# Optimization experiments

Measured on AMD Instinct MI355X. Metric: run time of the kernel, lower is better.

Reference implementation:

```python
import jax, jax.numpy as jnp
import numpy as np

TEMPERATURE = 0.5  # init temperature; attn_drop=0.0 so dropout is identity


def setup_inputs() -> dict:
    key = jax.random.key(0)
    k1, k2, k3 = jax.random.split(key, 3)
    B, H, N, D = 4, 8, 2048, 64
    q = jax.random.normal(k1, (B, H, N, D), dtype=jnp.float32)
    k = jax.random.normal(k2, (B, H, N, D), dtype=jnp.float32)
    v = jax.random.normal(k3, (B, H, N, D), dtype=jnp.float32)
    scale = jnp.asarray(D ** -0.5, dtype=jnp.float32)
    return {"q": q, "k": k, "v": v, "scale": scale}


def reference(q, k, v, scale):
    # logits: [B,H,N,N]
    logits = jnp.einsum("bhqd,bhkd->bhqk", q, k) * scale
    # first softmax acts as a soft mask over keys
    soft_mask = jax.nn.softmax(logits / TEMPERATURE, axis=-1)
    # second softmax over masked logits (elementwise product, NOT matmul)
    attn = jax.nn.softmax(logits * soft_mask, axis=-1)
    # dropout with p=0.0 is identity
    out = jnp.einsum("bhqk,bhkd->bhqd", attn, v)
    return out
```

## Files before the change

### kernel.cpp

```cpp
#include <hip/hip_runtime.h>


typedef _Float16 f16;
typedef f16 f16x8 __attribute__((ext_vector_type(8)));
typedef f16 f16x4 __attribute__((ext_vector_type(4)));
typedef float f32x4 __attribute__((ext_vector_type(4)));

#define MFMA32(a, b, c) __builtin_amdgcn_mfma_f32_16x16x32_f16((a), (b), (c), 0, 0, 0)
#define MFMA16(a, b, c) __builtin_amdgcn_mfma_f32_16x16x16f16((a), (b), (c), 0, 0, 0)
#define EXP2(x) __builtin_amdgcn_exp2f(x)

#define N_CTX 2048
#define DH 64
#define KT 64
#define NKT (N_CTX / KT)
#define ROWS 128
#define QS 72

#define C2 2.885390081777927f

__device__ inline unsigned pk(float a, float b) {
    typedef __fp16 fp16x2_t __attribute__((ext_vector_type(2)));
    union { fp16x2_t v; unsigned u; } x;
    x.v = __builtin_amdgcn_cvt_pkrtz(a, b);
    return x.u;
}

__global__ __launch_bounds__(512, 4)
void stk_attn_mfma(const float* __restrict__ qg, const float* __restrict__ kg,
                   const float* __restrict__ vglob, const float* __restrict__ sg,
                   float* __restrict__ og) {
    __shared__ f16 Ks[2][KT * QS];
    __shared__ f16 Vt[2][DH * QS];

    const int tid  = threadIdx.x;
    const int wv   = tid >> 6;
    const int lane = tid & 63;
    const int l15  = lane & 15;
    const int q4   = lane >> 4;
    const int vp   = tid & 31;
    const int vgr  = tid >> 5;
    const int bh   = blockIdx.x & 31;
    const int q0   = (blockIdx.x >> 5) * ROWS;
    const float scale2 = sg[0] * C2;

    const float* qb = qg + (size_t)bh * N_CTX * DH;
    const float* kb = kg + (size_t)bh * N_CTX * DH;
    const float* vb = vglob + (size_t)bh * N_CTX * DH;
    float*       ob = og + (size_t)bh * N_CTX * DH;

    f16x8 aq[2];
    {
        const float* qrow = qb + (size_t)(q0 + wv * 16 + l15) * DH;
        #pragma unroll
        for (int kc = 0; kc < 2; ++kc) {
            float4 a0 = *(const float4*)&qrow[kc * 32 + q4 * 8];
            float4 a1 = *(const float4*)&qrow[kc * 32 + q4 * 8 + 4];
            union { f16x8 h; unsigned u[4]; } A;
            A.u[0] = pk(a0.x * scale2, a0.y * scale2);
            A.u[1] = pk(a0.z * scale2, a0.w * scale2);
            A.u[2] = pk(a1.x * scale2, a1.y * scale2);
            A.u[3] = pk(a1.z * scale2, a1.w * scale2);
            aq[kc] = A.h;
        }
    }

    int kofs[2], gofs[2];
    #pragma unroll
    for (int it = 0; it < 2; ++it) {
        int idx = it * 512 + tid;
        gofs[it] = (idx >> 4) * DH + (idx & 15) * 4;
        kofs[it] = (idx >> 4) * QS + (idx & 15) * 4;
    }
    const int c2p = ((vp >> 1) & 3) * 16 + (vp >> 3) * 4 + (vp & 1) * 2;

    f16* const ks_w  = &Ks[0][0];
    const f16* const ks_r = &Ks[0][l15 * QS + q4 * 8];
    f16* const vt_w  = &Vt[0][(vgr * 4) * QS + c2p];
    const f16* const vt_r = &Vt[0][l15 * QS + q4 * 16];
    const int KSB = KT * QS;

    float s1 = 0.f;
    float4 kr[2];
    #pragma unroll
    for (int it = 0; it < 2; ++it)
        kr[it] = *(const float4*)&kb[gofs[it]];
    #pragma unroll
    for (int it = 0; it < 2; ++it)
        *(uint2*)&ks_w[kofs[it]] =
            make_uint2(pk(kr[it].x, kr[it].y), pk(kr[it].z, kr[it].w));
    #pragma unroll
    for (int it = 0; it < 2; ++it)
        kr[it] = *(const float4*)&kb[KT * DH + gofs[it]];
    __syncthreads();

    for (int kt = 0; kt < NKT; ++kt) {
        const int cur = (kt & 1) * KSB, nxt = KSB - cur;
        #pragma unroll
        for (int it = 0; it < 2; ++it)
            *(uint2*)&ks_w[nxt + kofs[it]] =
                make_uint2(pk(kr[it].x, kr[it].y), pk(kr[it].z, kr[it].w));
        {
            int tn = (kt + 2 < NKT) ? kt + 2 : NKT - 1;
            #pragma unroll
            for (int it = 0; it < 2; ++it)
                kr[it] = *(const float4*)&kb[(size_t)tn * KT * DH + gofs[it]];
        }
        __builtin_amdgcn_s_setprio(1);
        #pragma unroll
        for (int kgi = 0; kgi < 4; ++kgi) {
            f16x8 b0 = *(const f16x8*)&ks_r[cur + kgi * 16 * QS];
            f16x8 b1 = *(const f16x8*)&ks_r[cur + kgi * 16 * QS + 32];
            f32x4 acc = {0.f, 0.f, 0.f, 0.f};
            acc = MFMA32(b0, aq[0], acc);
            acc = MFMA32(b1, aq[1], acc);
            s1 += (EXP2(acc[0]) + EXP2(acc[1])) + (EXP2(acc[2]) + EXP2(acc[3]));
        }
        __builtin_amdgcn_s_setprio(0);
        __syncthreads();
    }
    s1 += __shfl_xor(s1, 16, 64);
    s1 += __shfl_xor(s1, 32, 64);
    const float inv1 = 0.5f / s1;

    f32x4 O[4];
    #pragma unroll
    for (int dt = 0; dt < 4; ++dt) O[dt] = (f32x4){0.f, 0.f, 0.f, 0.f};
    f32x4 Oe = {0.f, 0.f, 0.f, 0.f};
    const f16x4 ones = {(f16)1.f, (f16)1.f, (f16)1.f, (f16)1.f};

    float4 vr0, vr2;
    #pragma unroll
    for (int it = 0; it < 2; ++it)
        kr[it] = *(const float4*)&kb[gofs[it]];
    #pragma unroll
    for (int it = 0; it < 2; ++it)
        *(uint2*)&ks_w[kofs[it]] =
            make_uint2(pk(kr[it].x, kr[it].y), pk(kr[it].z, kr[it].w));
    {
        const float* vs = vb + ((size_t)2 * vp) * DH + vgr * 4;
        float4 a0 = *(const float4*)(vs);
        float4 b0 = *(const float4*)(vs + DH);
        #pragma unroll
        for (int j = 0; j < 4; ++j)
            *(unsigned*)&vt_w[j * QS] = pk(((const float*)&a0)[j], ((const float*)&b0)[j]);
        const float* vs1 = vb + ((size_t)(KT + 2 * vp)) * DH + vgr * 4;
        vr0 = *(const float4*)(vs1);
        vr2 = *(const float4*)(vs1 + DH);
    }
    #pragma unroll
    for (int it = 0; it < 2; ++it)
        kr[it] = *(const float4*)&kb[KT * DH + gofs[it]];
    __syncthreads();

    for (int kt = 0; kt < NKT; ++kt) {
        const int cur = (kt & 1) * KSB, nxt = KSB - cur;
        #pragma unroll
        for (int it = 0; it < 2; ++it)
            *(uint2*)&ks_w[nxt + kofs[it]] =
                make_uint2(pk(kr[it].x, kr[it].y), pk(kr[it].z, kr[it].w));
        #pragma unroll
        for (int j = 0; j < 4; ++j)
            *(unsigned*)&vt_w[nxt + j * QS] =
                pk(((const float*)&vr0)[j], ((const float*)&vr2)[j]);
        {
            int tn = (kt + 2 < NKT) ? kt + 2 : NKT - 1;
            #pragma unroll
            for (int it = 0; it < 2; ++it)
                kr[it] = *(const float4*)&kb[(size_t)tn * KT * DH + gofs[it]];
            const float* vs = vb + ((size_t)(tn * KT + 2 * vp)) * DH + vgr * 4;
            vr0 = *(const float4*)(vs);
            vr2 = *(const float4*)(vs + DH);
        }
        __builtin_amdgcn_s_setprio(1);
        #pragma unroll
        for (int p = 0; p < 2; ++p) {
            f16x4 pfr[2];
            #pragma unroll
            for (int h = 0; h < 2; ++h) {
                const int kgi = p * 2 + h;
                f16x8 b0 = *(const f16x8*)&ks_r[cur + kgi * 16 * QS];
                f16x8 b1 = *(const f16x8*)&ks_r[cur + kgi * 16 * QS + 32];
                f32x4 acc = {0.f, 0.f, 0.f, 0.f};
                acc = MFMA32(b0, aq[0], acc);
                acc = MFMA32(b1, aq[1], acc);
                float e2r[4];
                #pragma unroll
                for (int r = 0; r < 4; ++r) {
                    float a  = acc[r];
                    float e1 = EXP2(a);
                    e2r[r] = EXP2((a * e1) * inv1);
                }
                union { f16x4 hh; unsigned u[2]; } P;
                P.u[0] = pk(e2r[0], e2r[1]);
                P.u[1] = pk(e2r[2], e2r[3]);
                pfr[h] = P.hh;
                Oe = MFMA16(ones, pfr[h], Oe);
            }
            #pragma unroll
            for (int dt = 0; dt < 4; ++dt) {
                f16x8 av = *(const f16x8*)&vt_r[cur + dt * 16 * QS + p * 8];
                f16x4 alo = __builtin_shufflevector(av, av, 0, 1, 2, 3);
                f16x4 ahi = __builtin_shufflevector(av, av, 4, 5, 6, 7);
                O[dt] = MFMA16(alo, pfr[0], O[dt]);
                O[dt] = MFMA16(ahi, pfr[1], O[dt]);
            }
        }
        __builtin_amdgcn_s_setprio(0);
        __syncthreads();
    }

    const float invl2 = 1.0f / Oe[0];
    const size_t orow = (size_t)(q0 + wv * 16 + l15) * DH;
    #pragma unroll
    for (int dt = 0; dt < 4; ++dt) {
        float4 o;
        o.x = O[dt][0] * invl2;
        o.y = O[dt][1] * invl2;
        o.z = O[dt][2] * invl2;
        o.w = O[dt][3] * invl2;
        *(float4*)&ob[orow + dt * 16 + q4 * 4] = o;
    }
}

extern "C" void kernel_launch(void* const* d_in, const int* in_sizes, int n_in,
                              void* d_out, int out_size, void* d_ws, size_t ws_size,
                              hipStream_t stream) {
    const float* q = (const float*)d_in[0];
    const float* k = (const float*)d_in[1];
    const float* v = (const float*)d_in[2];
    const float* s = (const float*)d_in[3];
    float* out = (float*)d_out;
    dim3 grid(32 * 16);
    stk_attn_mfma<<<grid, 512, 0, stream>>>(q, k, v, s, out);
}
```

Baseline: 166.1 us.

## Split key range across two wave groups per block with LDS reduction

Measured after the change: 240.4 us. +44.7%, slower.

```diff
diff --git a/kernel.cpp b/kernel.cpp
--- a/kernel.cpp
+++ b/kernel.cpp
@@ -13,9 +13,11 @@
 #define N_CTX 2048
 #define DH 64
 #define KT 64
-#define NKT (N_CTX / KT)
+#define NKT_G 16
 #define ROWS 128
 #define QS 72
+#define KSB (KT * QS)
+#define SMEM_F16 (4 * 2 * KSB + 512)
 
 #define C2 2.885390081777927f
 
@@ -26,20 +28,22 @@
     return x.u;
 }
 
-__global__ __launch_bounds__(512, 4)
+__global__ __launch_bounds__(1024, 8)
 void stk_attn_mfma(const float* __restrict__ qg, const float* __restrict__ kg,
                    const float* __restrict__ vglob, const float* __restrict__ sg,
                    float* __restrict__ og) {
-    __shared__ f16 Ks[2][KT * QS];
-    __shared__ f16 Vt[2][DH * QS];
+    extern __shared__ f16 smem[];
 
     const int tid  = threadIdx.x;
     const int wv   = tid >> 6;
+    const int grp  = wv >> 3;
+    const int wv7  = wv & 7;
     const int lane = tid & 63;
     const int l15  = lane & 15;
     const int q4   = lane >> 4;
-    const int vp   = tid & 31;
-    const int vgr  = tid >> 5;
+    const int tg   = (wv7 << 6) | lane;
+    const int vp   = tg & 31;
+    const int vgr  = tg >> 5;
     const int bh   = blockIdx.x & 31;
     const int q0   = (blockIdx.x >> 5) * ROWS;
     const float scale2 = sg[0] * C2;
@@ -48,10 +52,12 @@
     const float* kb = kg + (size_t)bh * N_CTX * DH;
     const float* vb = vglob + (size_t)bh * N_CTX * DH;
     float*       ob = og + (size_t)bh * N_CTX * DH;
+    const float* kbg = kb + (size_t)grp * (NKT_G * KT) * DH;
+    const float* vbg = vb + (size_t)grp * (NKT_G * KT) * DH;
 
     f16x8 aq[2];
     {
-        const float* qrow = qb + (size_t)(q0 + wv * 16 + l15) * DH;
+        const float* qrow = qb + (size_t)(q0 + wv7 * 16 + l15) * DH;
         #pragma unroll
         for (int kc = 0; kc < 2; ++kc) {
             float4 a0 = *(const float4*)&qrow[kc * 32 + q4 * 8];
@@ -68,43 +74,47 @@
     int kofs[2], gofs[2];
     #pragma unroll
     for (int it = 0; it < 2; ++it) {
-        int idx = it * 512 + tid;
+        int idx = it * 512 + tg;
         gofs[it] = (idx >> 4) * DH + (idx & 15) * 4;
         kofs[it] = (idx >> 4) * QS + (idx & 15) * 4;
     }
     const int c2p = ((vp >> 1) & 3) * 16 + (vp >> 3) * 4 + (vp & 1) * 2;
 
-    f16* const ks_w  = &Ks[0][0];
-    const f16* const ks_r = &Ks[0][l15 * QS + q4 * 8];
-    f16* const vt_w  = &Vt[0][(vgr * 4) * QS + c2p];
-    const f16* const vt_r = &Vt[0][l15 * QS + q4 * 16];
-    const int KSB = KT * QS;
+    f16* const ksBase = smem + grp * (2 * KSB);
+    f16* const vtBase = smem + 2 * (2 * KSB) + grp * (2 * KSB);
+    float* const sred = (float*)(smem + 4 * (2 * KSB));
+    float* const obuf = (float*)smem;
+
+    f16* const ks_w  = ksBase;
+    const f16* const ks_r = ksBase + l15 * QS + q4 * 8;
+    f16* const vt_w  = vtBase + (vgr * 4) * QS + c2p;
+    const f16* const vt_r = vtBase + l15 * QS + q4 * 16;
 
     float s1 = 0.f;
     float4 kr[2];
     #pragma unroll
     for (int it = 0; it < 2; ++it)
-        kr[it] = *(const float4*)&kb[gofs[it]];
+        kr[it] = *(const float4*)&kbg[gofs[it]];
     #pragma unroll
     for (int it = 0; it < 2; ++it)
         *(uint2*)&ks_w[kofs[it]] =
             make_uint2(pk(kr[it].x, kr[it].y), pk(kr[it].z, kr[it].w));
     #pragma unroll
     for (int it = 0; it < 2; ++it)
-        kr[it] = *(const float4*)&kb[KT * DH + gofs[it]];
-    __syncthreads();
-
-    for (int kt = 0; kt < NKT; ++kt) {
+        kr[it] = *(const float4*)&kbg[KT * DH + gofs[it]];
+    __syncthreads();
+
+    for (int kt = 0; kt < NKT_G; ++kt) {
         const int cur = (kt & 1) * KSB, nxt = KSB - cur;
         #pragma unroll
         for (int it = 0; it < 2; ++it)
             *(uint2*)&ks_w[nxt + kofs[it]] =
                 make_uint2(pk(kr[it].x, kr[it].y), pk(kr[it].z, kr[it].w));
         {
-            int tn = (kt + 2 < NKT) ? kt + 2 : NKT - 1;
+            int tn = (kt + 2 < NKT_G) ? kt + 2 : NKT_G - 1;
             #pragma unroll
             for (int it = 0; it < 2; ++it)
-                kr[it] = *(const float4*)&kb[(size_t)tn * KT * DH + gofs[it]];
+                kr[it] = *(const float4*)&kbg[(size_t)tn * KT * DH + gofs[it]];
         }
         __builtin_amdgcn_s_setprio(1);
         #pragma unroll
@@ -121,6 +131,9 @@
     }
     s1 += __shfl_xor(s1, 16, 64);
     s1 += __shfl_xor(s1, 32, 64);
+    if (lane < 16) sred[(grp << 7) + (wv7 << 4) + lane] = s1;
+    __syncthreads();
+    s1 += sred[((grp ^ 1) << 7) + (wv7 << 4) + l15];
     const float inv1 = 0.5f / s1;
 
     f32x4 O[4];
@@ -132,28 +145,28 @@
     float4 vr0, vr2;
     #pragma unroll
     for (int it = 0; it < 2; ++it)
-        kr[it] = *(const float4*)&kb[gofs[it]];
+        kr[it] = *(const float4*)&kbg[gofs[it]];
     #pragma unroll
     for (int it = 0; it < 2; ++it)
         *(uint2*)&ks_w[kofs[it]] =
             make_uint2(pk(kr[it].x, kr[it].y), pk(kr[it].z, kr[it].w));
     {
-        const float* vs = vb + ((size_t)2 * vp) * DH + vgr * 4;
+        const float* vs = vbg + ((size_t)2 * vp) * DH + vgr * 4;
         float4 a0 = *(const float4*)(vs);
         float4 b0 = *(const float4*)(vs + DH);
         #pragma unroll
         for (int j = 0; j < 4; ++j)
             *(unsigned*)&vt_w[j * QS] = pk(((const float*)&a0)[j], ((const float*)&b0)[j]);
-        const float* vs1 = vb + ((size_t)(KT + 2 * vp)) * DH + vgr * 4;
+        const float* vs1 = vbg + ((size_t)(KT + 2 * vp)) * DH + vgr * 4;
         vr0 = *(const float4*)(vs1);
         vr2 = *(const float4*)(vs1 + DH);
     }
     #pragma unroll
     for (int it = 0; it < 2; ++it)
-        kr[it] = *(const float4*)&kb[KT * DH + gofs[it]];
-    __syncthreads();
-
-    for (int kt = 0; kt < NKT; ++kt) {
+        kr[it] = *(const float4*)&kbg[KT * DH + gofs[it]];
+    __syncthreads();
+
+    for (int kt = 0; kt < NKT_G; ++kt) {
         const int cur = (kt & 1) * KSB, nxt = KSB - cur;
         #pragma unroll
         for (int it = 0; it < 2; ++it)
@@ -164,11 +177,11 @@
             *(unsigned*)&vt_w[nxt + j * QS] =
                 pk(((const float*)&vr0)[j], ((const float*)&vr2)[j]);
         {
-            int tn = (kt + 2 < NKT) ? kt + 2 : NKT - 1;
+            int tn = (kt + 2 < NKT_G) ? kt + 2 : NKT_G - 1;
             #pragma unroll
             for (int it = 0; it < 2; ++it)
-                kr[it] = *(const float4*)&kb[(size_t)tn * KT * DH + gofs[it]];
-            const float* vs = vb + ((size_t)(tn * KT + 2 * vp)) * DH + vgr * 4;
+                kr[it] = *(const float4*)&kbg[(size_t)tn * KT * DH + gofs[it]];
+            const float* vs = vbg + ((size_t)(tn * KT + 2 * vp)) * DH + vgr * 4;
             vr0 = *(const float4*)(vs);
             vr2 = *(const float4*)(vs + DH);
         }
@@ -210,16 +223,29 @@
         __syncthreads();
     }
 
-    const float invl2 = 1.0f / Oe[0];
-    const size_t orow = (size_t)(q0 + wv * 16 + l15) * DH;
-    #pragma unroll
-    for (int dt = 0; dt < 4; ++dt) {
-        float4 o;
-        o.x = O[dt][0] * invl2;
-        o.y = O[dt][1] * invl2;
-        o.z = O[dt][2] * invl2;
-        o.w = O[dt][3] * invl2;
-        *(float4*)&ob[orow + dt * 16 + q4 * 4] = o;
+    const int rec = tg * 20;
+    if (grp) {
+        #pragma unroll
+        for (int dt = 0; dt < 4; ++dt)
+            *(f32x4*)&obuf[rec + dt * 4] = O[dt];
+        obuf[rec + 16] = Oe[0];
+    }
+    __syncthreads();
+    if (!grp) {
+        #pragma unroll
+        for (int dt = 0; dt < 4; ++dt)
+            O[dt] += *(const f32x4*)&obuf[rec + dt * 4];
+        const float invl2 = 1.0f / (Oe[0] + obuf[rec + 16]);
+        const size_t orow = (size_t)(q0 + wv7 * 16 + l15) * DH;
+        #pragma unroll
+        for (int dt = 0; dt < 4; ++dt) {
+            float4 o;
+            o.x = O[dt][0] * invl2;
+            o.y = O[dt][1] * invl2;
+            o.z = O[dt][2] * invl2;
+            o.w = O[dt][3] * invl2;
+            *(float4*)&ob[orow + dt * 16 + q4 * 4] = o;
+        }
     }
 }
 
@@ -232,5 +258,5 @@
     const float* s = (const float*)d_in[3];
     float* out = (float*)d_out;
     dim3 grid(32 * 16);
-    stk_attn_mfma<<<grid, 512, 0, stream>>>(q, k, v, s, out);
+    stk_attn_mfma<<<grid, 1024, SMEM_F16 * 2, stream>>>(q, k, v, s, out);
 }
```
